# Performance work log

Measured on AMD Instinct MI355X. Metric: run time of the kernel, lower is better.

The kernel has to match this reference:

```python
import jax, jax.numpy as jnp
import numpy as np

B, N, E, DJ, DE = 1024, 400, 128, 128, 128  # batch, nodes, edges, joint dim, edge dim (E must equal DJ and DE for BatchNorm1d on 3D input)
BN_EPS = 1e-5


def setup_inputs() -> dict:
    key = jax.random.key(0)
    ks = jax.random.split(key, 8)
    gout = jax.random.normal(ks[0], (B, N, DJ), dtype=jnp.float32)
    eout = jax.random.normal(ks[1], (B, E, DE), dtype=jnp.float32)
    start_shift = jax.random.uniform(ks[2], (B, E, N), dtype=jnp.float32)
    end_shift = jax.random.uniform(ks[3], (B, E, N), dtype=jnp.float32)
    # Linear params: nn.init.normal_(std=0.001), bias 0
    W1 = 0.001 * jax.random.normal(ks[4], (DJ, 2 * DJ), dtype=jnp.float32)
    b1 = jnp.zeros((DJ,), dtype=jnp.float32)
    W2 = 0.001 * jax.random.normal(ks[5], (DE, DJ), dtype=jnp.float32)
    b2 = jnp.zeros((DE,), dtype=jnp.float32)
    # BatchNorm affine params: weight=1, bias=0
    g1 = jnp.ones((DJ,), dtype=jnp.float32)
    beta1 = jnp.zeros((DJ,), dtype=jnp.float32)
    g2 = jnp.ones((DE,), dtype=jnp.float32)
    beta2 = jnp.zeros((DE,), dtype=jnp.float32)
    return {"gout": gout, "eout": eout, "start_shift": start_shift, "end_shift": end_shift,
            "W1": W1, "b1": b1, "W2": W2, "b2": b2,
            "g1": g1, "beta1": beta1, "g2": g2, "beta2": beta2}


def batchnorm1d(x, gamma, beta):
    # PyTorch BatchNorm1d on 3D input: channels at dim 1, biased variance over dims (0, 2)
    mean = jnp.mean(x, axis=(0, 2), keepdims=True)
    var = jnp.mean(jnp.square(x - mean), axis=(0, 2), keepdims=True)
    xhat = (x - mean) * jax.lax.rsqrt(var + BN_EPS)
    return xhat * gamma[None, :, None] + beta[None, :, None]


def reference(gout, eout, start_shift, end_shift, W1, b1, W2, b2, g1, beta1, g2, beta2):
    # node -> edge gather via dense shift matmuls: [B,E,N] @ [B,N,DJ] -> [B,E,DJ]
    start_nodes = jnp.matmul(start_shift, gout)
    end_nodes = jnp.matmul(end_shift, gout)
    x = jnp.concatenate([start_nodes, end_nodes], axis=2)  # [B, E, 2*DJ]
    h = jnp.einsum('bef,df->bed', x, W1) + b1  # Linear(2*DJ -> DJ)
    h = jax.nn.relu(batchnorm1d(h, g1, beta1))
    h = jnp.einsum('bed,od->beo', h, W2) + b2  # Linear(DJ -> DE)
    res = batchnorm1d(h, g2, beta2)
    return jax.nn.relu(eout + res)
```

## Files before the change

kernel.cpp:

```cpp
#include <hip/hip_runtime.h>
#include <stdint.h>

#define BB 1024
#define NN 400
#define EE 128
#define DD 128
#define NSLOT 64

typedef float f32x4 __attribute__((ext_vector_type(4)));
typedef short bf16x8 __attribute__((ext_vector_type(8)));
typedef short bf16x4 __attribute__((ext_vector_type(4)));

__device__ __forceinline__ short f2bf(float f) {
    uint32_t u = __builtin_bit_cast(uint32_t, f);
    u += 0x7fffu + ((u >> 16) & 1u);
    return (short)(u >> 16);
}

__device__ __forceinline__ bf16x8 cvt8(const f32x4 a, const f32x4 b) {
    bf16x8 r;
    r[0] = f2bf(a[0]); r[1] = f2bf(a[1]); r[2] = f2bf(a[2]); r[3] = f2bf(a[3]);
    r[4] = f2bf(b[0]); r[5] = f2bf(b[1]); r[6] = f2bf(b[2]); r[7] = f2bf(b[3]);
    return r;
}

__global__ __launch_bounds__(256, 3)
void k1_gemm(const float* __restrict__ gout, const float* __restrict__ ss,
             const float* __restrict__ es, const float* __restrict__ W1,
             const float* __restrict__ b1, float* __restrict__ h,
             float* __restrict__ stats1)
{
    __shared__ short As[128 * 40];
    __shared__ short Gs[128 * 40];
    __shared__ short Ps[128 * 128];

    const int bid = blockIdx.x;
    const int b   = bid >> 1;
    const int e0  = (bid & 1) * 64;
    const int t   = threadIdx.x;
    const int w   = t >> 6;
    const int l15 = t & 15;
    const int l4  = (t >> 4) & 3;

    f32x4 acc[2][8];
#pragma unroll
    for (int i = 0; i < 2; ++i)
#pragma unroll
        for (int j = 0; j < 8; ++j) acc[i][j] = f32x4{0.f, 0.f, 0.f, 0.f};

    f32x4 ar[4], gr[4];
    const int arow = t >> 3;
    const int acol = (t & 7) * 4;
    const int gkr  = t >> 5;
    const int gcol = (t & 31) * 4;

    auto load_tiles = [&](int k0) {
#pragma unroll
        for (int p = 0; p < 4; ++p) {
            int row = arow + 32 * p;
            int col = k0 + acol;
            const float* src = (row < 64)
                ? ss + (size_t)(b * EE + e0 + row) * NN + col
                : es + (size_t)(b * EE + e0 + row - 64) * NN + col;
            ar[p] = (col < NN) ? *(const f32x4*)src : f32x4{0.f, 0.f, 0.f, 0.f};
        }
#pragma unroll
        for (int p = 0; p < 4; ++p) {
            int kr = gkr + 8 * p;
            const float* src = gout + (size_t)(b * NN + k0 + kr) * DD + gcol;
            gr[p] = (k0 + kr < NN) ? *(const f32x4*)src : f32x4{0.f, 0.f, 0.f, 0.f};
        }
    };

    auto store_tiles = [&]() {
#pragma unroll
        for (int p = 0; p < 4; ++p) {
            int row = arow + 32 * p;
            bf16x4 v;
            v[0] = f2bf(ar[p][0]); v[1] = f2bf(ar[p][1]);
            v[2] = f2bf(ar[p][2]); v[3] = f2bf(ar[p][3]);
            *(bf16x4*)&As[row * 40 + acol] = v;
        }
#pragma unroll
        for (int p = 0; p < 4; ++p) {
            int kr = gkr + 8 * p;
            Gs[(gcol + 0) * 40 + kr] = f2bf(gr[p][0]);
            Gs[(gcol + 1) * 40 + kr] = f2bf(gr[p][1]);
            Gs[(gcol + 2) * 40 + kr] = f2bf(gr[p][2]);
            Gs[(gcol + 3) * 40 + kr] = f2bf(gr[p][3]);
        }
    };

    load_tiles(0);
    const int NK = (NN + 31) / 32;
    for (int step = 0; step < NK; ++step) {
        store_tiles();
        __syncthreads();
        if (step + 1 < NK) load_tiles((step + 1) * 32);
        bf16x8 af[2];
#pragma unroll
        for (int rf = 0; rf < 2; ++rf) {
            int row = w * 32 + rf * 16 + l15;
            af[rf] = *(const bf16x8*)&As[row * 40 + l4 * 8];
        }
#pragma unroll
        for (int cf = 0; cf < 8; ++cf) {
            int col = cf * 16 + l15;
            bf16x8 bfr = *(const bf16x8*)&Gs[col * 40 + l4 * 8];
            acc[0][cf] = __builtin_amdgcn_mfma_f32_16x16x32_bf16(af[0], bfr, acc[0][cf], 0, 0, 0);
            acc[1][cf] = __builtin_amdgcn_mfma_f32_16x16x32_bf16(af[1], bfr, acc[1][cf], 0, 0, 0);
        }
        __syncthreads();
    }

#pragma unroll
    for (int rf = 0; rf < 2; ++rf)
#pragma unroll
        for (int cf = 0; cf < 8; ++cf)
#pragma unroll
            for (int r = 0; r < 4; ++r) {
                int row = w * 32 + rf * 16 + l4 * 4 + r;
                int col = cf * 16 + l15;
                int off = row * 128 + (((col >> 3) ^ (row & 7)) * 8) + (col & 7);
                Ps[off] = f2bf(acc[rf][cf][r]);
            }
    __syncthreads();

    f32x4 hacc[4][2];
#pragma unroll
    for (int i = 0; i < 4; ++i) {
        hacc[i][0] = f32x4{0.f, 0.f, 0.f, 0.f};
        hacc[i][1] = f32x4{0.f, 0.f, 0.f, 0.f};
    }
#pragma unroll
    for (int kf = 0; kf < 8; ++kf) {
        const int k0   = kf * 32;
        const int roff = (kf >= 4) ? 64 : 0;
        const int cb   = ((k0 & 127) >> 3) + l4;
        bf16x8 af[4];
#pragma unroll
        for (int rf = 0; rf < 4; ++rf) {
            int row = roff + rf * 16 + l15;
            af[rf] = *(const bf16x8*)&Ps[row * 128 + ((cb ^ (row & 7)) * 8)];
        }
#pragma unroll
        for (int cf = 0; cf < 2; ++cf) {
            int j = w * 32 + cf * 16 + l15;
            const float* wp = W1 + (size_t)j * 256 + k0 + l4 * 8;
            bf16x8 bfr = cvt8(*(const f32x4*)wp, *(const f32x4*)(wp + 4));
#pragma unroll
            for (int rf = 0; rf < 4; ++rf)
                hacc[rf][cf] = __builtin_amdgcn_mfma_f32_16x16x32_bf16(af[rf], bfr, hacc[rf][cf], 0, 0, 0);
        }
    }

    float* red = (float*)As;
    const float bj0 = b1[w * 32 + l15];
    const float bj1 = b1[w * 32 + 16 + l15];
    const int j0 = w * 32 + l15;
#pragma unroll
    for (int rf = 0; rf < 4; ++rf) {
        f32x4 v0 = hacc[rf][0] + bj0;
        f32x4 v1 = hacc[rf][1] + bj1;
        int elb = rf * 16 + l4 * 4;
#pragma unroll
        for (int r = 0; r < 4; ++r) {
            float* hp = h + (size_t)(b * EE + e0 + elb + r) * DD;
            hp[j0]      = v0[r];
            hp[j0 + 16] = v1[r];
            float s = v0[r] + v1[r];
            float q = v0[r] * v0[r] + v1[r] * v1[r];
            s += __shfl_xor(s, 1); s += __shfl_xor(s, 2); s += __shfl_xor(s, 4); s += __shfl_xor(s, 8);
            q += __shfl_xor(q, 1); q += __shfl_xor(q, 2); q += __shfl_xor(q, 4); q += __shfl_xor(q, 8);
            if (l15 == 0) {
                red[(elb + r) * 4 + w]       = s;
                red[256 + (elb + r) * 4 + w] = q;
            }
        }
    }
    __syncthreads();
    if (t < 64) {
        float s = red[t * 4] + red[t * 4 + 1] + red[t * 4 + 2] + red[t * 4 + 3];
        float q = red[256 + t * 4] + red[256 + t * 4 + 1] + red[256 + t * 4 + 2] + red[256 + t * 4 + 3];
        int slot = bid & (NSLOT - 1);
        atomicAdd(&stats1[slot * 256 + e0 + t], s);
        atomicAdd(&stats1[slot * 256 + 128 + e0 + t], q);
    }
}

__global__ __launch_bounds__(256, 3)
void k3_gemm(const float* __restrict__ h, const float* __restrict__ W2,
             const float* __restrict__ b2, const float* __restrict__ g1,
             const float* __restrict__ bt1, float* __restrict__ out,
             const float* __restrict__ stats1, float* __restrict__ stats2)
{
    __shared__ short Xs[128 * 128];
    __shared__ float sc[128];
    __shared__ float sh[128];
    const int b   = blockIdx.x;
    const int t   = threadIdx.x;
    const int w   = t >> 6;
    const int l15 = t & 15;
    const int l4  = (t >> 4) & 3;

    if (t < 128) {
        float sm = 0.f, sq = 0.f;
#pragma unroll 8
        for (int sl = 0; sl < NSLOT; ++sl) {
            sm += stats1[sl * 256 + t];
            sq += stats1[sl * 256 + 128 + t];
        }
        const float inv_n = 1.0f / (1024.0f * 128.0f);
        float m    = sm * inv_n;
        float var  = sq * inv_n - m * m;
        float rstd = rsqrtf(var + 1e-5f);
        float s    = rstd * g1[t];
        sc[t] = s;
        sh[t] = bt1[t] - m * s;
    }
    __syncthreads();

    {
        const int eb = t >> 5;
        const int c4 = t & 31;
#pragma unroll
        for (int p = 0; p < 16; ++p) {
            int e = eb + 8 * p;
            f32x4 v = *(const f32x4*)(h + (size_t)(b * EE + e) * DD + c4 * 4);
            float s = sc[e], s0 = sh[e];
            bf16x4 o;
#pragma unroll
            for (int i = 0; i < 4; ++i)
                o[i] = f2bf(fmaxf(fmaf(v[i], s, s0), 0.0f));
            int col = c4 * 4;
            int off = e * 128 + (((col >> 3) ^ (e & 7)) * 8) + (col & 7);
            *(bf16x4*)&Xs[off] = o;
        }
    }
    __syncthreads();

    f32x4 acc[8][2];
#pragma unroll
    for (int i = 0; i < 8; ++i) {
        acc[i][0] = f32x4{0.f, 0.f, 0.f, 0.f};
        acc[i][1] = f32x4{0.f, 0.f, 0.f, 0.f};
    }
#pragma unroll
    for (int kf = 0; kf < 4; ++kf) {
        const int k0 = kf * 32;
        const int cb = (k0 >> 3) + l4;
        bf16x8 af[8];
#pragma unroll
        for (int rf = 0; rf < 8; ++rf) {
            int row = rf * 16 + l15;
            af[rf] = *(const bf16x8*)&Xs[row * 128 + ((cb ^ (row & 7)) * 8)];
        }
#pragma unroll
        for (int cf = 0; cf < 2; ++cf) {
            int j = w * 32 + cf * 16 + l15;
            const float* wp = W2 + (size_t)j * 128 + k0 + l4 * 8;
            bf16x8 bfr = cvt8(*(const f32x4*)wp, *(const f32x4*)(wp + 4));
#pragma unroll
            for (int rf = 0; rf < 8; ++rf)
                acc[rf][cf] = __builtin_amdgcn_mfma_f32_16x16x32_bf16(af[rf], bfr, acc[rf][cf], 0, 0, 0);
        }
    }

    __syncthreads();
    float* red = (float*)Xs;
    const float bj0 = b2[w * 32 + l15];
    const float bj1 = b2[w * 32 + 16 + l15];
    const int j0 = w * 32 + l15;
#pragma unroll
    for (int rf = 0; rf < 8; ++rf) {
        f32x4 v0 = acc[rf][0] + bj0;
        f32x4 v1 = acc[rf][1] + bj1;
        int elb = rf * 16 + l4 * 4;
#pragma unroll
        for (int r = 0; r < 4; ++r) {
            float* op = out + (size_t)(b * EE + elb + r) * DD;
            op[j0]      = v0[r];
            op[j0 + 16] = v1[r];
            float s = v0[r] + v1[r];
            float q = v0[r] * v0[r] + v1[r] * v1[r];
            s += __shfl_xor(s, 1); s += __shfl_xor(s, 2); s += __shfl_xor(s, 4); s += __shfl_xor(s, 8);
            q += __shfl_xor(q, 1); q += __shfl_xor(q, 2); q += __shfl_xor(q, 4); q += __shfl_xor(q, 8);
            if (l15 == 0) {
                red[(elb + r) * 4 + w]       = s;
                red[512 + (elb + r) * 4 + w] = q;
            }
        }
    }
    __syncthreads();
    if (t < 128) {
        float s = red[t * 4] + red[t * 4 + 1] + red[t * 4 + 2] + red[t * 4 + 3];
        float q = red[512 + t * 4] + red[512 + t * 4 + 1] + red[512 + t * 4 + 2] + red[512 + t * 4 + 3];
        int slot = b & (NSLOT - 1);
        atomicAdd(&stats2[slot * 256 + t], s);
        atomicAdd(&stats2[slot * 256 + 128 + t], q);
    }
}

__global__ __launch_bounds__(256)
void k5_final(const float* __restrict__ eout, const float* __restrict__ g2,
              const float* __restrict__ bt2, float* __restrict__ io,
              const float* __restrict__ stats2)
{
    __shared__ float sc[128];
    __shared__ float sh[128];
    const int t = threadIdx.x;
    if (t < 128) {
        float sm = 0.f, sq = 0.f;
#pragma unroll 8
        for (int sl = 0; sl < NSLOT; ++sl) {
            sm += stats2[sl * 256 + t];
            sq += stats2[sl * 256 + 128 + t];
        }
        const float inv_n = 1.0f / (1024.0f * 128.0f);
        float m    = sm * inv_n;
        float var  = sq * inv_n - m * m;
        float rstd = rsqrtf(var + 1e-5f);
        float s    = rstd * g2[t];
        sc[t] = s;
        sh[t] = bt2[t] - m * s;
    }
    __syncthreads();

    const int total4 = BB * EE * DD / 4;
    for (int i4 = blockIdx.x * blockDim.x + t; i4 < total4; i4 += gridDim.x * blockDim.x) {
        int e = (i4 >> 5) & 127;
        f32x4 v = *(f32x4*)(io + (size_t)i4 * 4);
        f32x4 u = *(const f32x4*)(eout + (size_t)i4 * 4);
        float s = sc[e], s0 = sh[e];
        f32x4 o;
#pragma unroll
        for (int i = 0; i < 4; ++i)
            o[i] = fmaxf(u[i] + fmaf(v[i], s, s0), 0.0f);
        *(f32x4*)(io + (size_t)i4 * 4) = o;
    }
}

extern "C" void kernel_launch(void* const* d_in, const int* in_sizes, int n_in,
                              void* d_out, int out_size, void* d_ws, size_t ws_size,
                              hipStream_t stream)
{
    const float* gout  = (const float*)d_in[0];
    const float* eout  = (const float*)d_in[1];
    const float* ss    = (const float*)d_in[2];
    const float* es    = (const float*)d_in[3];
    const float* W1    = (const float*)d_in[4];
    const float* b1    = (const float*)d_in[5];
    const float* W2    = (const float*)d_in[6];
    const float* b2    = (const float*)d_in[7];
    const float* g1    = (const float*)d_in[8];
    const float* bt1   = (const float*)d_in[9];
    const float* g2    = (const float*)d_in[10];
    const float* bt2   = (const float*)d_in[11];

    float* stats1 = (float*)d_ws;
    float* stats2 = stats1 + NSLOT * 256;
    float* h      = stats2 + NSLOT * 256;
    float* out    = (float*)d_out;

    hipMemsetAsync((void*)stats1, 0, 2 * NSLOT * 256 * sizeof(float), stream);
    k1_gemm<<<dim3(BB * 2), dim3(256), 0, stream>>>(gout, ss, es, W1, b1, h, stats1);
    k3_gemm<<<dim3(BB), dim3(256), 0, stream>>>(h, W2, b2, g1, bt1, out, stats1, stats2);
    k5_final<<<dim3(2048), dim3(256), 0, stream>>>(eout, g2, bt2, out, stats2);
}
```

Measured before the change: 269.2 us.

## Store intermediate h as bf16, swizzle G tile, alias LDS, raise occupancy

The intermediate h buffer is now written in bf16 rather than fp32, which halves the global traffic between k1 and k3. k3 reads it with 8-wide bf16 vector loads. The G tile transpose-store into shared memory now packs pairs of k values into 32-bit writes with an XOR swizzle, to reduce bank conflicts and cut the number of scalar LDS stores. Shared memory is aliased (Ps overlaps As/Gs) and launch bounds are raised to 4 blocks per CU for higher occupancy, at the cost of register pressure and an extra barrier. BN statistics still come from fp32 values, while the stored h is rounded to bf16.

```diff
diff --git a/kernel.cpp b/kernel.cpp
--- a/kernel.cpp
+++ b/kernel.cpp
@@ -8,6 +8,7 @@
 #define NSLOT 64
 
 typedef float f32x4 __attribute__((ext_vector_type(4)));
+typedef float f32x2 __attribute__((ext_vector_type(2)));
 typedef short bf16x8 __attribute__((ext_vector_type(8)));
 typedef short bf16x4 __attribute__((ext_vector_type(4)));
 
@@ -15,6 +16,10 @@
     uint32_t u = __builtin_bit_cast(uint32_t, f);
     u += 0x7fffu + ((u >> 16) & 1u);
     return (short)(u >> 16);
+}
+
+__device__ __forceinline__ float bf2f(short s) {
+    return __builtin_bit_cast(float, (uint32_t)((uint16_t)s) << 16);
 }
 
 __device__ __forceinline__ bf16x8 cvt8(const f32x4 a, const f32x4 b) {
@@ -24,15 +29,16 @@
     return r;
 }
 
-__global__ __launch_bounds__(256, 3)
+__global__ __launch_bounds__(256, 4)
 void k1_gemm(const float* __restrict__ gout, const float* __restrict__ ss,
              const float* __restrict__ es, const float* __restrict__ W1,
-             const float* __restrict__ b1, float* __restrict__ h,
+             const float* __restrict__ b1, unsigned short* __restrict__ h,
              float* __restrict__ stats1)
 {
-    __shared__ short As[128 * 40];
-    __shared__ short Gs[128 * 40];
-    __shared__ short Ps[128 * 128];
+    __shared__ short lds[16384];
+    short* As = lds;
+    short* Gs = lds + 5120;
+    short* Ps = lds;
 
     const int bid = blockIdx.x;
     const int b   = bid >> 1;
@@ -48,13 +54,14 @@
 #pragma unroll
         for (int j = 0; j < 8; ++j) acc[i][j] = f32x4{0.f, 0.f, 0.f, 0.f};
 
-    f32x4 ar[4], gr[4];
+    f32x4 ar[4];
     const int arow = t >> 3;
     const int acol = (t & 7) * 4;
-    const int gkr  = t >> 5;
-    const int gcol = (t & 31) * 4;
-
-    auto load_tiles = [&](int k0) {
+    f32x2 g0[4], g1[4];
+    const int gx = t & 31;
+    const int gk = (t >> 5) * 2;
+
+    auto load_a = [&](int k0) {
 #pragma unroll
         for (int p = 0; p < 4; ++p) {
             int row = arow + 32 * p;
@@ -64,15 +71,18 @@
                 : es + (size_t)(b * EE + e0 + row - 64) * NN + col;
             ar[p] = (col < NN) ? *(const f32x4*)src : f32x4{0.f, 0.f, 0.f, 0.f};
         }
+    };
+    auto load_g = [&](int k0) {
 #pragma unroll
         for (int p = 0; p < 4; ++p) {
-            int kr = gkr + 8 * p;
-            const float* src = gout + (size_t)(b * NN + k0 + kr) * DD + gcol;
-            gr[p] = (k0 + kr < NN) ? *(const f32x4*)src : f32x4{0.f, 0.f, 0.f, 0.f};
+            int d0 = 2 * gx + 64 * (p & 1);
+            int k  = k0 + gk + 16 * (p >> 1);
+            const float* base = gout + (size_t)b * NN * DD + (size_t)k * DD + d0;
+            g0[p] = (k < NN)     ? *(const f32x2*)base        : f32x2{0.f, 0.f};
+            g1[p] = (k + 1 < NN) ? *(const f32x2*)(base + DD) : f32x2{0.f, 0.f};
         }
     };
-
-    auto store_tiles = [&]() {
+    auto store_a = [&]() {
 #pragma unroll
         for (int p = 0; p < 4; ++p) {
             int row = arow + 32 * p;
@@ -81,22 +91,29 @@
             v[2] = f2bf(ar[p][2]); v[3] = f2bf(ar[p][3]);
             *(bf16x4*)&As[row * 40 + acol] = v;
         }
+    };
+    auto store_g = [&]() {
 #pragma unroll
         for (int p = 0; p < 4; ++p) {
-            int kr = gkr + 8 * p;
-            Gs[(gcol + 0) * 40 + kr] = f2bf(gr[p][0]);
-            Gs[(gcol + 1) * 40 + kr] = f2bf(gr[p][1]);
-            Gs[(gcol + 2) * 40 + kr] = f2bf(gr[p][2]);
-            Gs[(gcol + 3) * 40 + kr] = f2bf(gr[p][3]);
+            int d0 = 2 * gx + 64 * (p & 1);
+            int kp = gk + 16 * (p >> 1);
+            uint32_t lo = (uint32_t)(uint16_t)f2bf(g0[p][0]) |
+                          ((uint32_t)(uint16_t)f2bf(g1[p][0]) << 16);
+            uint32_t hi = (uint32_t)(uint16_t)f2bf(g0[p][1]) |
+                          ((uint32_t)(uint16_t)f2bf(g1[p][1]) << 16);
+            int c  = (kp >> 3) ^ ((d0 >> 2) & 3);
+            int a0 = d0 * 40 + (c << 3) + (kp & 7);
+            *(uint32_t*)&Gs[a0]      = lo;
+            *(uint32_t*)&Gs[a0 + 40] = hi;
         }
     };
 
-    load_tiles(0);
+    load_a(0); load_g(0);
     const int NK = (NN + 31) / 32;
     for (int step = 0; step < NK; ++step) {
-        store_tiles();
+        store_a(); store_g();
         __syncthreads();
-        if (step + 1 < NK) load_tiles((step + 1) * 32);
+        if (step + 1 < NK) { load_a((step + 1) * 32); load_g((step + 1) * 32); }
         bf16x8 af[2];
 #pragma unroll
         for (int rf = 0; rf < 2; ++rf) {
@@ -106,7 +123,8 @@
 #pragma unroll
         for (int cf = 0; cf < 8; ++cf) {
             int col = cf * 16 + l15;
-            bf16x8 bfr = *(const bf16x8*)&Gs[col * 40 + l4 * 8];
+            int cc  = l4 ^ ((col >> 2) & 3);
+            bf16x8 bfr = *(const bf16x8*)&Gs[col * 40 + cc * 8];
             acc[0][cf] = __builtin_amdgcn_mfma_f32_16x16x32_bf16(af[0], bfr, acc[0][cf], 0, 0, 0);
             acc[1][cf] = __builtin_amdgcn_mfma_f32_16x16x32_bf16(af[1], bfr, acc[1][cf], 0, 0, 0);
         }
@@ -153,8 +171,9 @@
                 hacc[rf][cf] = __builtin_amdgcn_mfma_f32_16x16x32_bf16(af[rf], bfr, hacc[rf][cf], 0, 0, 0);
         }
     }
-
-    float* red = (float*)As;
+    __syncthreads();
+
+    float* red = (float*)lds;
     const float bj0 = b1[w * 32 + l15];
     const float bj1 = b1[w * 32 + 16 + l15];
     const int j0 = w * 32 + l15;
@@ -165,9 +184,9 @@
         int elb = rf * 16 + l4 * 4;
 #pragma unroll
         for (int r = 0; r < 4; ++r) {
-            float* hp = h + (size_t)(b * EE + e0 + elb + r) * DD;
-            hp[j0]      = v0[r];
-            hp[j0 + 16] = v1[r];
+            unsigned short* hp = h + (size_t)(b * EE + e0 + elb + r) * DD;
+            hp[j0]      = (unsigned short)f2bf(v0[r]);
+            hp[j0 + 16] = (unsigned short)f2bf(v1[r]);
             float s = v0[r] + v1[r];
             float q = v0[r] * v0[r] + v1[r] * v1[r];
             s += __shfl_xor(s, 1); s += __shfl_xor(s, 2); s += __shfl_xor(s, 4); s += __shfl_xor(s, 8);
@@ -188,8 +207,8 @@
     }
 }
 
-__global__ __launch_bounds__(256, 3)
-void k3_gemm(const float* __restrict__ h, const float* __restrict__ W2,
+__global__ __launch_bounds__(256, 4)
+void k3_gemm(const unsigned short* __restrict__ h, const float* __restrict__ W2,
              const float* __restrict__ b2, const float* __restrict__ g1,
              const float* __restrict__ bt1, float* __restrict__ out,
              const float* __restrict__ stats1, float* __restrict__ stats2)
@@ -221,20 +240,18 @@
     __syncthreads();
 
     {
-        const int eb = t >> 5;
-        const int c4 = t & 31;
-#pragma unroll
-        for (int p = 0; p < 16; ++p) {
-            int e = eb + 8 * p;
-            f32x4 v = *(const f32x4*)(h + (size_t)(b * EE + e) * DD + c4 * 4);
+        const int c8 = t & 15;
+        const int eb = t >> 4;
+#pragma unroll
+        for (int p = 0; p < 8; ++p) {
+            int e = eb + 16 * p;
+            bf16x8 v8 = *(const bf16x8*)&h[((size_t)b * EE + e) * DD + c8 * 8];
             float s = sc[e], s0 = sh[e];
-            bf16x4 o;
-#pragma unroll
-            for (int i = 0; i < 4; ++i)
-                o[i] = f2bf(fmaxf(fmaf(v[i], s, s0), 0.0f));
-            int col = c4 * 4;
-            int off = e * 128 + (((col >> 3) ^ (e & 7)) * 8) + (col & 7);
-            *(bf16x4*)&Xs[off] = o;
+            bf16x8 o;
+#pragma unroll
+            for (int i = 0; i < 8; ++i)
+                o[i] = f2bf(fmaxf(fmaf(bf2f(v8[i]), s, s0), 0.0f));
+            *(bf16x8*)&Xs[e * 128 + ((c8 ^ (e & 7)) << 3)] = o;
         }
     }
     __syncthreads();
@@ -359,7 +376,7 @@
 
     float* stats1 = (float*)d_ws;
     float* stats2 = stats1 + NSLOT * 256;
-    float* h      = stats2 + NSLOT * 256;
+    unsigned short* h = (unsigned short*)(stats2 + NSLOT * 256);
     float* out    = (float*)d_out;
 
     hipMemsetAsync((void*)stats1, 0, 2 * NSLOT * 256 * sizeof(float), stream);
```

Measured after the change: 258.0 us. 1.04x faster.
